# Kernel tuning notes

Measured on AMD Instinct MI355X. Metric: run time of the kernel, lower is better.

The kernel has to match this reference:

```python
import jax, jax.numpy as jnp
import numpy as np

N = 8192      # nodes
E = 8192      # target edges
H = 256       # in_channels == hidden_channels (required by module structure)
OUT = 1
ADJ_P = 0.004 # ~33 avg degree


def _linear_params(key, din, dout):
    kw, kb = jax.random.split(key)
    s = 1.0 / np.sqrt(din)
    w = jax.random.uniform(kw, (din, dout), jnp.float32, -s, s)
    b = jax.random.uniform(kb, (dout,), jnp.float32, -s, s)
    return w, b


def setup_inputs() -> dict:
    key = jax.random.key(0)
    ks = jax.random.split(key, 10)
    x = jax.random.normal(ks[0], (N, H), jnp.float32)
    # binary adjacency (symmetric not required by the math)
    adj = (jax.random.uniform(ks[1], (N, N)) < ADJ_P).astype(jnp.float32)
    tar_ei = jax.random.randint(ks[2], (2, E), 0, N)
    xlin_w, xlin_b = _linear_params(ks[3], H, H)
    xcnlin_w, xcnlin_b = _linear_params(ks[4], H, H)
    xijlini_w, xijlini_b = _linear_params(ks[5], H, H)
    xijlinj_w, xijlinj_b = _linear_params(ks[6], H, H)
    xijfinal_w, xijfinal_b = _linear_params(ks[7], H, H)
    xslin_w, xslin_b = _linear_params(ks[8], H, OUT)
    beta = jnp.ones((1,), jnp.float32)
    return {
        'x': x, 'adj': adj, 'tar_ei': tar_ei,
        'xlin_w': xlin_w, 'xlin_b': xlin_b,
        'xcnlin_w': xcnlin_w, 'xcnlin_b': xcnlin_b,
        'xijlini_w': xijlini_w, 'xijlini_b': xijlini_b,
        'xijlinj_w': xijlinj_w, 'xijlinj_b': xijlinj_b,
        'xijfinal_w': xijfinal_w, 'xijfinal_b': xijfinal_b,
        'xslin_w': xslin_w, 'xslin_b': xslin_b,
        'beta': beta, 'boolen': 1,
    }


def reference(x, adj, tar_ei, xlin_w, xlin_b, xcnlin_w, xcnlin_b,
              xijlini_w, xijlini_b, xijlinj_w, xijlinj_b,
              xijfinal_w, xijfinal_b, xslin_w, xslin_b, beta, boolen):
    src, dst = tar_ei[0], tar_ei[1]
    xi = x[src]                       # [E,H]
    xj = x[dst]                       # [E,H]
    x2 = x + (x @ xlin_w + xlin_b)    # x = x + xlin(x)
    # adjoverlap: common-neighbor indicator per target edge = A[i] AND A[j]
    cn = adj[src] * adj[dst]          # [E,N] binary mask
    xcn = cn @ x2                     # spmm_add(cn, x) -> [E,H]
    xij = jax.nn.relu((xi @ xijlini_w + xijlini_b) + (xj @ xijlinj_w + xijlinj_b))
    xij = xij @ xijfinal_w + xijfinal_b
    xs = (xcn @ xcnlin_w + xcnlin_b) * beta + xij
    # NOTE: source's `xs.relu()` result is discarded (not in-place) -> no relu
    xs = xs @ xslin_w + xslin_b       # [E,OUT]
    sign = 1.0 if boolen else -1.0
    return -jax.nn.log_sigmoid(sign * xs)
```

## Files before the change

### kernel.cpp

```cpp
#include <hip/hip_runtime.h>
#include <hip/hip_bf16.h>

#define Nn 8192
#define Ee 8192
#define Hh 256
#define MASK_W 128

typedef unsigned long long u64;

__global__ void __launch_bounds__(256)
preA_kernel(const float* __restrict__ Wc, const float* __restrict__ Wf,
            const float* __restrict__ v_, const float* __restrict__ bc,
            const float* __restrict__ bf_, const float* __restrict__ bs,
            const float* __restrict__ beta, const int* __restrict__ boolen,
            float* __restrict__ u, float* __restrict__ w2,
            float* __restrict__ consts) {
    const int tid = threadIdx.x;
    if (blockIdx.x < 64) {
        const int wave = tid >> 6;
        const int lane = tid & 63;
        const int k = blockIdx.x * 4 + wave;
        float a = 0.f, b = 0.f;
#pragma unroll
        for (int i = 0; i < 4; ++i) {
            const int j = lane + 64 * i;
            const float vv = v_[j];
            a = fmaf(Wc[k * Hh + j], vv, a);
            b = fmaf(Wf[k * Hh + j], vv, b);
        }
        for (int off = 32; off > 0; off >>= 1) {
            a += __shfl_down(a, off);
            b += __shfl_down(b, off);
        }
        if (lane == 0) { u[k] = a; w2[k] = b; }
        return;
    }
    __shared__ float red[Hh];
    __shared__ float red2[Hh];
    const float vv = v_[tid];
    red[tid]  = bc[tid]  * vv;
    red2[tid] = bf_[tid] * vv;
    __syncthreads();
    for (int s = 128; s > 0; s >>= 1) {
        if (tid < s) { red[tid] += red[tid + s]; red2[tid] += red2[tid + s]; }
        __syncthreads();
    }
    if (tid == 0) {
        const float be = beta[0];
        consts[1] = be * red[0] + red2[0] + bs[0];
        consts[2] = (boolen[0] != 0) ? 1.f : -1.f;
        consts[3] = be;
    }
}

__global__ void __launch_bounds__(256)
preB_kernel(const float* __restrict__ Wx, const float* __restrict__ bx,
            const float* __restrict__ u, float* __restrict__ g,
            float* __restrict__ consts) {
    const int tid = threadIdx.x;
    if (blockIdx.x < 64) {
        const int wave = tid >> 6;
        const int lane = tid & 63;
        const int k = blockIdx.x * 4 + wave;
        float a = 0.f;
#pragma unroll
        for (int i = 0; i < 4; ++i) {
            const int j = lane + 64 * i;
            a = fmaf(Wx[k * Hh + j], u[j], a);
        }
        for (int off = 32; off > 0; off >>= 1) a += __shfl_down(a, off);
        if (lane == 0) g[k] = u[k] + a;
        return;
    }
    __shared__ float red[Hh];
    red[tid] = bx[tid] * u[tid];
    __syncthreads();
    for (int s = 128; s > 0; s >>= 1) { if (tid < s) red[tid] += red[tid + s]; __syncthreads(); }
    if (tid == 0) consts[0] = red[0];
}

__global__ void __launch_bounds__(256)
pack_kernel(const float* __restrict__ adj, u64* __restrict__ mask) {
    const int wave_id = blockIdx.x * 4 + (threadIdx.x >> 6);
    const int lane = threadIdx.x & 63;
    const int row  = wave_id >> 1;
    const int half = wave_id & 1;
    const float4* src = reinterpret_cast<const float4*>(
        adj + (size_t)row * Nn + half * 4096);

    u64 myword = 0;
#pragma unroll
    for (int i = 0; i < 16; ++i) {
        const float4 v = src[i * 64 + lane];
        unsigned int nib = 0;
        nib |= (v.x != 0.f) ? 1u : 0u;
        nib |= (v.y != 0.f) ? 2u : 0u;
        nib |= (v.z != 0.f) ? 4u : 0u;
        nib |= (v.w != 0.f) ? 8u : 0u;
        const unsigned int t1 = __shfl_xor(nib, 1);
        const unsigned int by = nib | (t1 << 4);
        const unsigned int t2 = __shfl_xor(by, 2);
        const unsigned int h16 = by | (t2 << 8);
        const unsigned int t4 = __shfl_xor(h16, 4);
        const unsigned int w32 = h16 | (t4 << 16);
        const unsigned int t8 = __shfl_xor(w32, 8);
        const u64 w64 = (u64)w32 | ((u64)t8 << 32);
        const u64 got = __shfl(w64, (lane & 3) << 4);
        if ((lane >> 2) == i) myword = got;
    }
    mask[(size_t)row * MASK_W + half * 64 + lane] = myword;
}

#define RQ 16
__global__ void __launch_bounds__(256)
pq_kernel(const float* __restrict__ x,
          const float* __restrict__ Wi, const float* __restrict__ Wj,
          const float* __restrict__ bi, const float* __restrict__ bj,
          const float* __restrict__ g, const float* __restrict__ consts,
          float* __restrict__ P, float* __restrict__ Q, float* __restrict__ t) {
    __shared__ float xs[RQ][Hh];
    const int tid = threadIdx.x;
    const int base = blockIdx.x * RQ;

    {
        const float4* xv = reinterpret_cast<const float4*>(x + (size_t)base * Hh);
        float4* xd = reinterpret_cast<float4*>(&xs[0][0]);
#pragma unroll
        for (int i = tid; i < 1024; i += 256) xd[i] = xv[i];
    }
    __syncthreads();

    {
        const int wave = tid >> 6;
        const int lane = tid & 63;
        const float c0 = consts[0];
#pragma unroll
        for (int r0 = 0; r0 < 4; ++r0) {
            const int r = wave * 4 + r0;
            float s = 0.f;
#pragma unroll
            for (int i = 0; i < 4; ++i) {
                const int c = lane * 4 + i;
                s = fmaf(xs[r][c], g[c], s);
            }
            for (int off = 32; off > 0; off >>= 1) s += __shfl_down(s, off);
            if (lane == 0) t[base + r] = s + c0;
        }
    }

    float accP[RQ], accQ[RQ];
    const float fbi = bi[tid], fbj = bj[tid];
#pragma unroll
    for (int r = 0; r < RQ; ++r) { accP[r] = fbi; accQ[r] = fbj; }

#pragma unroll 4
    for (int k = 0; k < Hh; ++k) {
        const float wiv = Wi[k * Hh + tid];
        const float wjv = Wj[k * Hh + tid];
#pragma unroll
        for (int r = 0; r < RQ; ++r) {
            accP[r] = fmaf(xs[r][k], wiv, accP[r]);
            accQ[r] = fmaf(xs[r][k], wjv, accQ[r]);
        }
    }
#pragma unroll
    for (int r = 0; r < RQ; ++r) {
        P[(size_t)(base + r) * Hh + tid] = accP[r];
        Q[(size_t)(base + r) * Hh + tid] = accQ[r];
    }
}

__global__ void edge_kernel(const u64* __restrict__ mask, const int* __restrict__ tei,
                            const float* __restrict__ P, const float* __restrict__ Q,
                            const float* __restrict__ w2, const float* __restrict__ t,
                            const float* __restrict__ consts, float* __restrict__ out) {
    const int e = blockIdx.x;
    const int tid = threadIdx.x;
    const int src = tei[e];
    const int dst = tei[Ee + e];

    __shared__ u64 ms[MASK_W];
    __shared__ u64 md[MASK_W];
    if (tid < MASK_W) ms[tid] = mask[(size_t)src * MASK_W + tid];
    else              md[tid - MASK_W] = mask[(size_t)dst * MASK_W + (tid - MASK_W)];
    __syncthreads();

    float accA = 0.f;
    if (tid < MASK_W) {
        u64 m = ms[tid] & md[tid];
        while (m) {
            const int b = __builtin_ctzll(m);
            accA += t[tid * 64 + b];
            m &= m - 1;
        }
    }
    const float r = P[(size_t)src * Hh + tid] + Q[(size_t)dst * Hh + tid];
    float accB = (r > 0.f) ? r * w2[tid] : 0.f;

    for (int off = 32; off > 0; off >>= 1) {
        accA += __shfl_down(accA, off);
        accB += __shfl_down(accB, off);
    }
    __shared__ float wA[4], wB[4];
    const int wave = tid >> 6;
    if ((tid & 63) == 0) { wA[wave] = accA; wB[wave] = accB; }
    __syncthreads();
    if (tid == 0) {
        const float sA = wA[0] + wA[1] + wA[2] + wA[3];
        const float sB = wB[0] + wB[1] + wB[2] + wB[3];
        const float be = consts[3];
        const float sgn = consts[2];
        const float s = be * sA + sB + consts[1];
        const float m = -sgn * s;
        const float res = fmaxf(m, 0.f) + log1pf(expf(-fabsf(m)));
        out[e] = res;
    }
}

extern "C" void kernel_launch(void* const* d_in, const int* in_sizes, int n_in,
                              void* d_out, int out_size, void* d_ws, size_t ws_size,
                              hipStream_t stream) {
    const float* x     = (const float*)d_in[0];
    const float* adj   = (const float*)d_in[1];
    const int*   tei   = (const int*)d_in[2];
    const float* Wx    = (const float*)d_in[3];
    const float* bx    = (const float*)d_in[4];
    const float* Wc    = (const float*)d_in[5];
    const float* bc    = (const float*)d_in[6];
    const float* Wi    = (const float*)d_in[7];
    const float* bi    = (const float*)d_in[8];
    const float* Wj    = (const float*)d_in[9];
    const float* bj    = (const float*)d_in[10];
    const float* Wf    = (const float*)d_in[11];
    const float* bf_   = (const float*)d_in[12];
    const float* v_    = (const float*)d_in[13];
    const float* bs    = (const float*)d_in[14];
    const float* beta  = (const float*)d_in[15];
    const int*   booln = (const int*)d_in[16];
    float* out = (float*)d_out;

    float* u      = (float*)d_ws;
    float* w2     = u + 256;
    float* g      = w2 + 256;
    float* consts = g + 256;
    float* t      = consts + 8;
    float* P      = t + 8192;
    float* Q      = P + (size_t)Nn * Hh;
    u64*   mask   = (u64*)(Q + (size_t)Nn * Hh);

    pack_kernel<<<(Nn * 2) / 4, 256, 0, stream>>>(adj, mask);
    preA_kernel<<<65, 256, 0, stream>>>(Wc, Wf, v_, bc, bf_, bs, beta, booln,
                                        u, w2, consts);
    preB_kernel<<<65, 256, 0, stream>>>(Wx, bx, u, g, consts);
    pq_kernel<<<Nn / RQ, 256, 0, stream>>>(x, Wi, Wj, bi, bj, g, consts, P, Q, t);
    edge_kernel<<<Ee, 256, 0, stream>>>(mask, tei, P, Q, w2, t, consts, out);
}
```

Measured before the change: 527.6 us.

## Merge precompute kernels and fuse adjacency packing with PQ projection launch

The two small precompute kernels become one single-block kernel that computes u, w2, g and the scalar constants with per-thread row dot products. The adjacency bit-packing work is folded into the same launch as the P/Q projection, using extra blocks, so the two independent workloads can overlap on the GPU. Adjacency loads now use nontemporal loads to avoid polluting cache. This cuts launch count and lets the bandwidth-bound packing overlap compute. The cost is a serial single-block precompute with strided per-thread row reads.

```diff
diff --git a/kernel.cpp b/kernel.cpp
--- a/kernel.cpp
+++ b/kernel.cpp
@@ -1,127 +1,118 @@
 #include <hip/hip_runtime.h>
-#include <hip/hip_bf16.h>
 
 #define Nn 8192
 #define Ee 8192
 #define Hh 256
 #define MASK_W 128
+#define RQ 16
+#define NPQ 512
 
 typedef unsigned long long u64;
+typedef float nf4 __attribute__((ext_vector_type(4)));
 
 __global__ void __launch_bounds__(256)
-preA_kernel(const float* __restrict__ Wc, const float* __restrict__ Wf,
-            const float* __restrict__ v_, const float* __restrict__ bc,
-            const float* __restrict__ bf_, const float* __restrict__ bs,
-            const float* __restrict__ beta, const int* __restrict__ boolen,
-            float* __restrict__ u, float* __restrict__ w2,
-            float* __restrict__ consts) {
+pre_kernel(const float* __restrict__ Wc, const float* __restrict__ Wf,
+           const float* __restrict__ Wx, const float* __restrict__ v_,
+           const float* __restrict__ bc, const float* __restrict__ bf_,
+           const float* __restrict__ bx, const float* __restrict__ bs,
+           const float* __restrict__ beta, const int* __restrict__ boolen,
+           float* __restrict__ w2, float* __restrict__ g,
+           float* __restrict__ consts) {
+    __shared__ float sv[Hh];
+    __shared__ float su[Hh];
+    __shared__ float r1[Hh], r2[Hh], r3[Hh];
     const int tid = threadIdx.x;
-    if (blockIdx.x < 64) {
-        const int wave = tid >> 6;
-        const int lane = tid & 63;
-        const int k = blockIdx.x * 4 + wave;
-        float a = 0.f, b = 0.f;
-#pragma unroll
-        for (int i = 0; i < 4; ++i) {
-            const int j = lane + 64 * i;
-            const float vv = v_[j];
-            a = fmaf(Wc[k * Hh + j], vv, a);
-            b = fmaf(Wf[k * Hh + j], vv, b);
-        }
-        for (int off = 32; off > 0; off >>= 1) {
-            a += __shfl_down(a, off);
-            b += __shfl_down(b, off);
-        }
-        if (lane == 0) { u[k] = a; w2[k] = b; }
-        return;
-    }
-    __shared__ float red[Hh];
-    __shared__ float red2[Hh];
-    const float vv = v_[tid];
-    red[tid]  = bc[tid]  * vv;
-    red2[tid] = bf_[tid] * vv;
+    sv[tid] = v_[tid];
+    __syncthreads();
+
+    const float4* wc4 = reinterpret_cast<const float4*>(Wc + (size_t)tid * Hh);
+    const float4* wf4 = reinterpret_cast<const float4*>(Wf + (size_t)tid * Hh);
+    const float4* sv4 = reinterpret_cast<const float4*>(sv);
+    float a = 0.f, b = 0.f;
+#pragma unroll 8
+    for (int j = 0; j < Hh / 4; ++j) {
+        const float4 w = wc4[j];
+        const float4 f = wf4[j];
+        const float4 s = sv4[j];
+        a = fmaf(w.x, s.x, fmaf(w.y, s.y, fmaf(w.z, s.z, fmaf(w.w, s.w, a))));
+        b = fmaf(f.x, s.x, fmaf(f.y, s.y, fmaf(f.z, s.z, fmaf(f.w, s.w, b))));
+    }
+    su[tid] = a;
+    w2[tid] = b;
+    __syncthreads();
+
+    const float4* wx4 = reinterpret_cast<const float4*>(Wx + (size_t)tid * Hh);
+    const float4* su4 = reinterpret_cast<const float4*>(su);
+    float c = a;
+#pragma unroll 8
+    for (int j = 0; j < Hh / 4; ++j) {
+        const float4 w = wx4[j];
+        const float4 uu = su4[j];
+        c = fmaf(w.x, uu.x, fmaf(w.y, uu.y, fmaf(w.z, uu.z, fmaf(w.w, uu.w, c))));
+    }
+    g[tid] = c;
+
+    r1[tid] = bc[tid] * sv[tid];
+    r2[tid] = bf_[tid] * sv[tid];
+    r3[tid] = bx[tid] * a;
     __syncthreads();
     for (int s = 128; s > 0; s >>= 1) {
-        if (tid < s) { red[tid] += red[tid + s]; red2[tid] += red2[tid + s]; }
+        if (tid < s) { r1[tid] += r1[tid + s]; r2[tid] += r2[tid + s]; r3[tid] += r3[tid + s]; }
         __syncthreads();
     }
     if (tid == 0) {
         const float be = beta[0];
-        consts[1] = be * red[0] + red2[0] + bs[0];
+        consts[0] = r3[0];
+        consts[1] = be * r1[0] + r2[0] + bs[0];
         consts[2] = (boolen[0] != 0) ? 1.f : -1.f;
         consts[3] = be;
     }
 }
 
 __global__ void __launch_bounds__(256)
-preB_kernel(const float* __restrict__ Wx, const float* __restrict__ bx,
-            const float* __restrict__ u, float* __restrict__ g,
-            float* __restrict__ consts) {
-    const int tid = threadIdx.x;
-    if (blockIdx.x < 64) {
-        const int wave = tid >> 6;
-        const int lane = tid & 63;
-        const int k = blockIdx.x * 4 + wave;
-        float a = 0.f;
-#pragma unroll
-        for (int i = 0; i < 4; ++i) {
-            const int j = lane + 64 * i;
-            a = fmaf(Wx[k * Hh + j], u[j], a);
-        }
-        for (int off = 32; off > 0; off >>= 1) a += __shfl_down(a, off);
-        if (lane == 0) g[k] = u[k] + a;
-        return;
-    }
-    __shared__ float red[Hh];
-    red[tid] = bx[tid] * u[tid];
-    __syncthreads();
-    for (int s = 128; s > 0; s >>= 1) { if (tid < s) red[tid] += red[tid + s]; __syncthreads(); }
-    if (tid == 0) consts[0] = red[0];
-}
-
-__global__ void __launch_bounds__(256)
-pack_kernel(const float* __restrict__ adj, u64* __restrict__ mask) {
-    const int wave_id = blockIdx.x * 4 + (threadIdx.x >> 6);
-    const int lane = threadIdx.x & 63;
-    const int row  = wave_id >> 1;
-    const int half = wave_id & 1;
-    const float4* src = reinterpret_cast<const float4*>(
-        adj + (size_t)row * Nn + half * 4096);
-
-    u64 myword = 0;
-#pragma unroll
-    for (int i = 0; i < 16; ++i) {
-        const float4 v = src[i * 64 + lane];
-        unsigned int nib = 0;
-        nib |= (v.x != 0.f) ? 1u : 0u;
-        nib |= (v.y != 0.f) ? 2u : 0u;
-        nib |= (v.z != 0.f) ? 4u : 0u;
-        nib |= (v.w != 0.f) ? 8u : 0u;
-        const unsigned int t1 = __shfl_xor(nib, 1);
-        const unsigned int by = nib | (t1 << 4);
-        const unsigned int t2 = __shfl_xor(by, 2);
-        const unsigned int h16 = by | (t2 << 8);
-        const unsigned int t4 = __shfl_xor(h16, 4);
-        const unsigned int w32 = h16 | (t4 << 16);
-        const unsigned int t8 = __shfl_xor(w32, 8);
-        const u64 w64 = (u64)w32 | ((u64)t8 << 32);
-        const u64 got = __shfl(w64, (lane & 3) << 4);
-        if ((lane >> 2) == i) myword = got;
-    }
-    mask[(size_t)row * MASK_W + half * 64 + lane] = myword;
-}
-
-#define RQ 16
-__global__ void __launch_bounds__(256)
-pq_kernel(const float* __restrict__ x,
-          const float* __restrict__ Wi, const float* __restrict__ Wj,
-          const float* __restrict__ bi, const float* __restrict__ bj,
-          const float* __restrict__ g, const float* __restrict__ consts,
-          float* __restrict__ P, float* __restrict__ Q, float* __restrict__ t) {
+fusedA_kernel(const float* __restrict__ adj, u64* __restrict__ mask,
+              const float* __restrict__ x,
+              const float* __restrict__ Wi, const float* __restrict__ Wj,
+              const float* __restrict__ bi, const float* __restrict__ bj,
+              const float* __restrict__ g, const float* __restrict__ consts,
+              float* __restrict__ P, float* __restrict__ Q,
+              float* __restrict__ t) {
     __shared__ float xs[RQ][Hh];
     const int tid = threadIdx.x;
+
+    if (blockIdx.x >= NPQ) {
+        const int wave_id = (blockIdx.x - NPQ) * 4 + (tid >> 6);
+        const int lane = tid & 63;
+        const int row  = wave_id >> 1;
+        const int half = wave_id & 1;
+        const nf4* src = reinterpret_cast<const nf4*>(
+            adj + (size_t)row * Nn + half * 4096);
+
+        u64 myword = 0;
+#pragma unroll
+        for (int i = 0; i < 16; ++i) {
+            const nf4 v = __builtin_nontemporal_load(src + i * 64 + lane);
+            unsigned int nib = 0;
+            nib |= (v.x != 0.f) ? 1u : 0u;
+            nib |= (v.y != 0.f) ? 2u : 0u;
+            nib |= (v.z != 0.f) ? 4u : 0u;
+            nib |= (v.w != 0.f) ? 8u : 0u;
+            const unsigned int t1 = __shfl_xor(nib, 1);
+            const unsigned int by = nib | (t1 << 4);
+            const unsigned int t2 = __shfl_xor(by, 2);
+            const unsigned int h16 = by | (t2 << 8);
+            const unsigned int t4 = __shfl_xor(h16, 4);
+            const unsigned int w32 = h16 | (t4 << 16);
+            const unsigned int t8 = __shfl_xor(w32, 8);
+            const u64 w64 = (u64)w32 | ((u64)t8 << 32);
+            const u64 got = __shfl(w64, (lane & 3) << 4);
+            if ((lane >> 2) == i) myword = got;
+        }
+        mask[(size_t)row * MASK_W + half * 64 + lane] = myword;
+        return;
+    }
+
     const int base = blockIdx.x * RQ;
-
     {
         const float4* xv = reinterpret_cast<const float4*>(x + (size_t)base * Hh);
         float4* xd = reinterpret_cast<float4*>(&xs[0][0]);
@@ -239,8 +230,7 @@
     const int*   booln = (const int*)d_in[16];
     float* out = (float*)d_out;
 
-    float* u      = (float*)d_ws;
-    float* w2     = u + 256;
+    float* w2     = (float*)d_ws;
     float* g      = w2 + 256;
     float* consts = g + 256;
     float* t      = consts + 8;
@@ -248,10 +238,10 @@
     float* Q      = P + (size_t)Nn * Hh;
     u64*   mask   = (u64*)(Q + (size_t)Nn * Hh);
 
-    pack_kernel<<<(Nn * 2) / 4, 256, 0, stream>>>(adj, mask);
-    preA_kernel<<<65, 256, 0, stream>>>(Wc, Wf, v_, bc, bf_, bs, beta, booln,
-                                        u, w2, consts);
-    preB_kernel<<<65, 256, 0, stream>>>(Wx, bx, u, g, consts);
-    pq_kernel<<<Nn / RQ, 256, 0, stream>>>(x, Wi, Wj, bi, bj, g, consts, P, Q, t);
+    pre_kernel<<<1, 256, 0, stream>>>(Wc, Wf, Wx, v_, bc, bf_, bx, bs, beta,
+                                      booln, w2, g, consts);
+    fusedA_kernel<<<NPQ + (Nn * 2) / 4, 256, 0, stream>>>(adj, mask, x, Wi, Wj,
+                                                          bi, bj, g, consts,
+                                                          P, Q, t);
     edge_kernel<<<Ee, 256, 0, stream>>>(mask, tei, P, Q, w2, t, consts, out);
 }
```

Result: faster. 447.7 us (-15.1%).
